# Kernel optimization log

Measured on AMD Instinct MI355X. Metric: run time of the kernel, lower is better.

## Reference

```python
import jax, jax.numpy as jnp
import numpy as np

DN = ('NCHW', 'HWIO', 'NCHW')

def conv_same(x, w):
    # TF 'same' padding for even kernels pads more at the end; lax 'SAME' matches.
    return jax.lax.conv_general_dilated(x, w, (1, 1), 'SAME', dimension_numbers=DN)

def hard_sigmoid(z):
    # Keras hard_sigmoid
    return jnp.clip(0.2 * z + 0.5, 0.0, 1.0)

def setup_inputs() -> dict:
    key = jax.random.key(0)
    k1, k2, k3 = jax.random.split(key, 3)
    B, T, C, H, W = 8, 16, 16, 128, 128
    FILTERS = 2
    x = jax.random.normal(k1, (B, T, C, H, W), jnp.float32)
    # Keras HWIO kernels; 4*filters output channels for i,f,c,o gates
    Wx = jax.random.normal(k2, (4, 2, C, 4 * FILTERS), jnp.float32) * 0.05
    Wh = jax.random.normal(k3, (4, 2, FILTERS, 4 * FILTERS), jnp.float32) * 0.05
    return {"x": x, "Wx": Wx, "Wh": Wh}

def convlstm(x, Wx, Wh):
    B, T, C, H, W = x.shape
    F = Wh.shape[2]  # filters
    # go_backwards=True: process time axis reversed; outputs stay in processed order
    xr = x[:, ::-1]
    # Precompute input convolution for all timesteps in one big conv
    xg = conv_same(xr.reshape(B * T, C, H, W), Wx).reshape(B, T, 4 * F, H, W)
    xg = jnp.moveaxis(xg, 1, 0)  # (T, B, 4F, H, W)
    h0 = jnp.zeros((B, F, H, W), x.dtype)
    c0 = jnp.zeros((B, F, H, W), x.dtype)

    def step(carry, xg_t):
        h, c = carry
        hg = conv_same(h, Wh)  # (B, 4F, H, W)
        xi, xf, xc, xo = jnp.split(xg_t, 4, axis=1)
        hi, hf, hc, ho = jnp.split(hg, 4, axis=1)
        i = hard_sigmoid(xi + hi)
        f = hard_sigmoid(xf + hf)
        c_new = f * c + i * jnp.tanh(xc + hc)
        o = hard_sigmoid(xo + ho)
        h_new = o * jnp.tanh(c_new)
        return (h_new, c_new), h_new

    _, hs = jax.lax.scan(step, (h0, c0), xg)  # hs: (T, B, F, H, W)
    return jnp.moveaxis(hs, 0, 1)  # (B, T, F, H, W)

def reference(x, Wx, Wh):
    return convlstm(x, Wx, Wh)
```

## Files before the change

### kernel.cpp

```cpp
#include <hip/hip_runtime.h>
#include <cmath>


constexpr int B_ = 8;
constexpr int T_ = 16;
constexpr int C_ = 16;
constexpr int F_ = 2;
constexpr int O_ = 8;
constexpr int H_ = 128;
constexpr int W_ = 128;
constexpr int HW_ = H_ * W_;
constexpr int KH_ = 4;
constexpr int KW_ = 2;
constexpr int PX_ = 4;

typedef float fv4 __attribute__((ext_vector_type(4)));

__device__ __forceinline__ float hsig(float z) {
    return fminf(fmaxf(0.2f * z + 0.5f, 0.0f), 1.0f);
}

__device__ __forceinline__ float ftanh(float x) {
    float e = __expf(2.0f * x);
    return fmaf(-2.0f, 1.0f / (e + 1.0f), 1.0f);
}

template<bool CHECK>
__device__ __forceinline__ void load4(
    const float* __restrict__ xc,
    int r0m1, fv4 a[KH_])
{
    #pragma unroll
    for (int rr = 0; rr < KH_; ++rr) {
        int ih = r0m1 + rr;
        if (CHECK) {
            bool v = (unsigned)ih < (unsigned)H_;
            a[rr] = *reinterpret_cast<const fv4*>(xc + (v ? ih : 0) * W_);
            if (!v) a[rr] = (fv4)0.0f;
        } else {
            a[rr] = *reinterpret_cast<const fv4*>(xc + ih * W_);
        }
    }
}

__device__ __forceinline__ void accum4(
    const float* __restrict__ wc,
    const fv4 a[KH_], float acc[PX_][O_], bool cval)
{
    #pragma unroll
    for (int kh = 0; kh < KH_; ++kh) {
        float x4 = __shfl_down(a[kh].x, 1, 64);
        x4 = cval ? x4 : 0.0f;
        const float* wp = wc + kh * (KW_ * C_ * O_);
        #pragma unroll
        for (int o = 0; o < O_; ++o) {
            float w0 = wp[o];
            float w1 = wp[C_ * O_ + o];
            acc[0][o] = fmaf(a[kh].x, w0, acc[0][o]);
            acc[1][o] = fmaf(a[kh].y, w0, acc[1][o]);
            acc[2][o] = fmaf(a[kh].z, w0, acc[2][o]);
            acc[3][o] = fmaf(a[kh].w, w0, acc[3][o]);
            acc[0][o] = fmaf(a[kh].y, w1, acc[0][o]);
            acc[1][o] = fmaf(a[kh].z, w1, acc[1][o]);
            acc[2][o] = fmaf(a[kh].w, w1, acc[2][o]);
            acc[3][o] = fmaf(x4,      w1, acc[3][o]);
        }
    }
}

template<bool CHECK>
__device__ __forceinline__ void conv_pipe(
    const float* __restrict__ xb,
    const float* __restrict__ Wx,
    int r0m1, bool cval, float acc[PX_][O_])
{
    fv4 A[KH_], Bv[KH_];
    load4<CHECK>(xb, r0m1, A);
    #pragma unroll 1
    for (int cc = 0; cc < C_ - 2; cc += 2) {
        load4<CHECK>(xb + (cc + 1) * HW_, r0m1, Bv);
        accum4(Wx + cc * O_, A, acc, cval);
        load4<CHECK>(xb + (cc + 2) * HW_, r0m1, A);
        accum4(Wx + (cc + 1) * O_, Bv, acc, cval);
    }
    load4<CHECK>(xb + (C_ - 1) * HW_, r0m1, Bv);
    accum4(Wx + (C_ - 2) * O_, A, acc, cval);
    accum4(Wx + (C_ - 1) * O_, Bv, acc, cval);
}

__global__ __launch_bounds__(256, 4) void xg_kernel(
    const float* __restrict__ x,
    const float* __restrict__ Wx,
    float* __restrict__ xg)
{
    int wid = (blockIdx.x & 7) * 256 + (blockIdx.x >> 3);

    int bt   = wid >> 4;
    int slab = wid & 15;

    int tid = threadIdx.x;
    int oh_l = tid >> 5;
    int q    = tid & 31;
    int ow4  = q << 2;

    int r0 = slab * 8 + oh_l;

    int b    = bt >> 4;
    int trev = bt & 15;
    int t    = 15 - trev;

    const float* xb = x + (size_t)bt * C_ * HW_ + ow4;
    bool cval = ow4 < (W_ - 4);

    float acc[PX_][O_];
    #pragma unroll
    for (int p = 0; p < PX_; ++p)
        #pragma unroll
        for (int o = 0; o < O_; ++o) acc[p][o] = 0.0f;

    if (slab >= 1 && slab <= 14) {
        conv_pipe<false>(xb, Wx, r0 - 1, cval, acc);
    } else {
        conv_pipe<true>(xb, Wx, r0 - 1, cval, acc);
    }

    float* dst = xg + (size_t)(t * B_ + b) * O_ * HW_ + r0 * W_ + ow4;
    #pragma unroll
    for (int o = 0; o < O_; ++o) {
        fv4 s;
        s.x = acc[0][o]; s.y = acc[1][o]; s.z = acc[2][o]; s.w = acc[3][o];
        __builtin_nontemporal_store(s, reinterpret_cast<fv4*>(dst + o * HW_));
    }
}

__global__ __launch_bounds__(256) void step_kernel(
    const float* __restrict__ xg,
    const float* __restrict__ Wh,
    float* __restrict__ out,
    float* __restrict__ cbuf,
    int t)
{
    int gid = blockIdx.x * 256 + threadIdx.x;
    int b   = gid >> 14;
    int pix = gid & (HW_ - 1);
    int oh  = pix >> 7;
    int ow  = pix & (W_ - 1);

    const float* xgp = xg + (size_t)(t * B_ + b) * O_ * HW_ + pix;
    float acc[O_];
    #pragma unroll
    for (int o = 0; o < O_; ++o)
        acc[o] = __builtin_nontemporal_load(xgp + o * HW_);

    bool cv  = (ow + 1) < W_;
    int  co1 = cv ? 1 : 0;

    if (t > 0) {
        const float* hs = out + (size_t)(b * T_ + (t - 1)) * F_ * HW_;
        #pragma unroll
        for (int kh = 0; kh < KH_; ++kh) {
            int ih  = oh + kh - 1;
            bool rv = (unsigned)ih < (unsigned)H_;
            int ihc = rv ? ih : 0;
            const float* hrow = hs + ihc * W_ + ow;
            const float* wb   = Wh + kh * (KW_ * F_ * O_);
            #pragma unroll
            for (int f = 0; f < F_; ++f) {
                float h0 = hrow[f * HW_];
                float h1 = hrow[f * HW_ + co1];
                h0 = rv ? h0 : 0.0f;
                h1 = (rv && cv) ? h1 : 0.0f;
                #pragma unroll
                for (int o = 0; o < O_; ++o) {
                    acc[o] = fmaf(h0, wb[f * O_ + o], acc[o]);
                    acc[o] = fmaf(h1, wb[F_ * O_ + f * O_ + o], acc[o]);
                }
            }
        }
    }

    size_t cidx = (size_t)b * F_ * HW_ + pix;
    float cp0 = 0.0f, cp1 = 0.0f;
    if (t > 0) { cp0 = cbuf[cidx]; cp1 = cbuf[cidx + HW_]; }

    float gi0 = hsig(acc[0]);
    float gi1 = hsig(acc[1]);
    float gf0 = hsig(acc[2]);
    float gf1 = hsig(acc[3]);
    float gg0 = ftanh(acc[4]);
    float gg1 = ftanh(acc[5]);
    float go0 = hsig(acc[6]);
    float go1 = hsig(acc[7]);

    float cn0 = gf0 * cp0 + gi0 * gg0;
    float cn1 = gf1 * cp1 + gi1 * gg1;
    cbuf[cidx]       = cn0;
    cbuf[cidx + HW_] = cn1;

    size_t oidx = (size_t)(b * T_ + t) * F_ * HW_ + pix;
    out[oidx]       = go0 * ftanh(cn0);
    out[oidx + HW_] = go1 * ftanh(cn1);
}

extern "C" void kernel_launch(void* const* d_in, const int* in_sizes, int n_in,
                              void* d_out, int out_size, void* d_ws, size_t ws_size,
                              hipStream_t stream) {
    const float* x  = (const float*)d_in[0];
    const float* Wx = (const float*)d_in[1];
    const float* Wh = (const float*)d_in[2];
    float* out  = (float*)d_out;

    float* xg   = (float*)d_ws;
    float* cbuf = (float*)((char*)d_ws + (size_t)64 * 1024 * 1024 + 1024);

    int xg_blocks = (B_ * T_ * HW_ / PX_) / 256;
    xg_kernel<<<xg_blocks, 256, 0, stream>>>(x, Wx, xg);

    int blocks = (B_ * HW_) / 256;
    for (int t = 0; t < T_; ++t) {
        step_kernel<<<blocks, 256, 0, stream>>>(xg, Wh, out, cbuf, t);
    }
}
```

Baseline: 118.9 us.

## Split step kernel threads per output filter and deepen xg load pipeline

The step kernel now assigns one thread per (pixel, output filter) instead of one per pixel. This doubles the thread count, and each thread computes 4 gate accumulators instead of 8. The change is meant to raise parallelism and cut per-thread work in the latency-bound recurrent steps, at the cost of loading the hidden state twice. The xg convolution's input pipeline also moves from double to quad buffering of channel loads, which adds more loads in flight but also more register pressure.

New measurement: 208.5 us. +75.3%, slower.

```diff
diff --git a/kernel.cpp b/kernel.cpp
--- a/kernel.cpp
+++ b/kernel.cpp
@@ -74,18 +74,21 @@
     const float* __restrict__ Wx,
     int r0m1, bool cval, float acc[PX_][O_])
 {
-    fv4 A[KH_], Bv[KH_];
-    load4<CHECK>(xb, r0m1, A);
+    fv4 A[KH_], Bv[KH_], Cv[KH_], Dv[KH_];
+    load4<CHECK>(xb,        r0m1, A);
+    load4<CHECK>(xb + HW_,  r0m1, Bv);
     #pragma unroll 1
-    for (int cc = 0; cc < C_ - 2; cc += 2) {
-        load4<CHECK>(xb + (cc + 1) * HW_, r0m1, Bv);
+    for (int g = 0; g < 4; ++g) {
+        int cc = g * 4;
+        load4<CHECK>(xb + (cc + 2) * HW_, r0m1, Cv);
         accum4(Wx + cc * O_, A, acc, cval);
-        load4<CHECK>(xb + (cc + 2) * HW_, r0m1, A);
+        load4<CHECK>(xb + (cc + 3) * HW_, r0m1, Dv);
         accum4(Wx + (cc + 1) * O_, Bv, acc, cval);
-    }
-    load4<CHECK>(xb + (C_ - 1) * HW_, r0m1, Bv);
-    accum4(Wx + (C_ - 2) * O_, A, acc, cval);
-    accum4(Wx + (C_ - 1) * O_, Bv, acc, cval);
+        if (cc + 4 < C_) load4<CHECK>(xb + (cc + 4) * HW_, r0m1, A);
+        accum4(Wx + (cc + 2) * O_, Cv, acc, cval);
+        if (cc + 5 < C_) load4<CHECK>(xb + (cc + 5) * HW_, r0m1, Bv);
+        accum4(Wx + (cc + 3) * O_, Dv, acc, cval);
+    }
 }
 
 __global__ __launch_bounds__(256, 4) void xg_kernel(
@@ -98,7 +101,7 @@
     int bt   = wid >> 4;
     int slab = wid & 15;
 
-    int tid = threadIdx.x;
+    int tid  = threadIdx.x;
     int oh_l = tid >> 5;
     int q    = tid & 31;
     int ow4  = q << 2;
@@ -140,17 +143,18 @@
     float* __restrict__ cbuf,
     int t)
 {
-    int gid = blockIdx.x * 256 + threadIdx.x;
-    int b   = gid >> 14;
-    int pix = gid & (HW_ - 1);
-    int oh  = pix >> 7;
-    int ow  = pix & (W_ - 1);
-
-    const float* xgp = xg + (size_t)(t * B_ + b) * O_ * HW_ + pix;
-    float acc[O_];
-    #pragma unroll
-    for (int o = 0; o < O_; ++o)
-        acc[o] = __builtin_nontemporal_load(xgp + o * HW_);
+    int tid = threadIdx.x;
+    int f   = tid >> 7;
+    int ow  = tid & 127;
+    int oh  = blockIdx.x & 127;
+    int b   = blockIdx.x >> 7;
+    int pix = oh * W_ + ow;
+
+    const float* xgp = xg + ((size_t)(t * B_ + b) * O_ + f) * HW_ + pix;
+    float a_i = __builtin_nontemporal_load(xgp);
+    float a_f = __builtin_nontemporal_load(xgp + 2 * HW_);
+    float a_g = __builtin_nontemporal_load(xgp + 4 * HW_);
+    float a_o = __builtin_nontemporal_load(xgp + 6 * HW_);
 
     bool cv  = (ow + 1) < W_;
     int  co1 = cv ? 1 : 0;
@@ -163,43 +167,32 @@
             bool rv = (unsigned)ih < (unsigned)H_;
             int ihc = rv ? ih : 0;
             const float* hrow = hs + ihc * W_ + ow;
-            const float* wb   = Wh + kh * (KW_ * F_ * O_);
             #pragma unroll
-            for (int f = 0; f < F_; ++f) {
-                float h0 = hrow[f * HW_];
-                float h1 = hrow[f * HW_ + co1];
+            for (int fin = 0; fin < F_; ++fin) {
+                float h0 = hrow[fin * HW_];
+                float h1 = hrow[fin * HW_ + co1];
                 h0 = rv ? h0 : 0.0f;
                 h1 = (rv && cv) ? h1 : 0.0f;
-                #pragma unroll
-                for (int o = 0; o < O_; ++o) {
-                    acc[o] = fmaf(h0, wb[f * O_ + o], acc[o]);
-                    acc[o] = fmaf(h1, wb[F_ * O_ + f * O_ + o], acc[o]);
-                }
+                const float* wb = Wh + kh * (KW_ * F_ * O_) + fin * O_ + f;
+                a_i = fmaf(h0, wb[0],  a_i);  a_i = fmaf(h1, wb[16], a_i);
+                a_f = fmaf(h0, wb[2],  a_f);  a_f = fmaf(h1, wb[18], a_f);
+                a_g = fmaf(h0, wb[4],  a_g);  a_g = fmaf(h1, wb[20], a_g);
+                a_o = fmaf(h0, wb[6],  a_o);  a_o = fmaf(h1, wb[22], a_o);
             }
         }
     }
 
-    size_t cidx = (size_t)b * F_ * HW_ + pix;
-    float cp0 = 0.0f, cp1 = 0.0f;
-    if (t > 0) { cp0 = cbuf[cidx]; cp1 = cbuf[cidx + HW_]; }
-
-    float gi0 = hsig(acc[0]);
-    float gi1 = hsig(acc[1]);
-    float gf0 = hsig(acc[2]);
-    float gf1 = hsig(acc[3]);
-    float gg0 = ftanh(acc[4]);
-    float gg1 = ftanh(acc[5]);
-    float go0 = hsig(acc[6]);
-    float go1 = hsig(acc[7]);
-
-    float cn0 = gf0 * cp0 + gi0 * gg0;
-    float cn1 = gf1 * cp1 + gi1 * gg1;
-    cbuf[cidx]       = cn0;
-    cbuf[cidx + HW_] = cn1;
-
-    size_t oidx = (size_t)(b * T_ + t) * F_ * HW_ + pix;
-    out[oidx]       = go0 * ftanh(cn0);
-    out[oidx + HW_] = go1 * ftanh(cn1);
+    float gi = hsig(a_i);
+    float gf = hsig(a_f);
+    float gg = ftanh(a_g);
+    float go = hsig(a_o);
+
+    size_t cidx = (size_t)b * F_ * HW_ + (size_t)f * HW_ + pix;
+    float cp = (t > 0) ? cbuf[cidx] : 0.0f;
+    float cn = gf * cp + gi * gg;
+    cbuf[cidx] = cn;
+
+    out[(size_t)(b * T_ + t) * F_ * HW_ + (size_t)f * HW_ + pix] = go * ftanh(cn);
 }
 
 extern "C" void kernel_launch(void* const* d_in, const int* in_sizes, int n_in,
@@ -216,8 +209,8 @@
     int xg_blocks = (B_ * T_ * HW_ / PX_) / 256;
     xg_kernel<<<xg_blocks, 256, 0, stream>>>(x, Wx, xg);
 
-    int blocks = (B_ * HW_) / 256;
+    int step_blocks = B_ * H_;
     for (int t = 0; t < T_; ++t) {
-        step_kernel<<<blocks, 256, 0, stream>>>(xg, Wh, out, cbuf, t);
-    }
-}
+        step_kernel<<<step_blocks, 256, 0, stream>>>(xg, Wh, out, cbuf, t);
+    }
+}
```
